# Optimization experiments

Hardware: AMD Instinct MI355X
Metric: run time of the kernel (lower is better)

The kernel has to match this reference:

```python
import jax, jax.numpy as jnp
import numpy as np

N_ETYPES = 4


def setup_inputs() -> dict:
    key = jax.random.key(0)
    ks = jax.random.split(key, 6)
    N, E, F = 50000, 800000, 128
    x = jax.random.normal(ks[0], (N, F), dtype=jnp.float32)
    edge_index = jax.random.randint(ks[1], (2, E), 0, N, dtype=jnp.int64)
    edge_type = jax.random.randint(ks[2], (E,), 0, N_ETYPES, dtype=jnp.int64)
    scale = 1.0 / np.sqrt(F)
    W_self = jax.random.normal(ks[3], (N_ETYPES, F, F), dtype=jnp.float32) * scale
    W_neigh = jax.random.normal(ks[4], (N_ETYPES, F, F), dtype=jnp.float32) * scale
    b = jnp.zeros((N_ETYPES, F), dtype=jnp.float32)
    return {"x": x, "edge_index": edge_index, "edge_type": edge_type,
            "W_self": W_self, "W_neigh": W_neigh, "b": b}


def reference(x, edge_index, edge_type, W_self, W_neigh, b):
    # HeteroConv: per-edge-type SageConv (mean aggregation), then mean over types.
    N = x.shape[0]
    src, dst = edge_index[0], edge_index[1]
    msg = x[src]                                   # [E, F] gathered source features
    outs = []
    for t in range(N_ETYPES):                      # small fixed loop over edge types
        w = (edge_type == t).astype(x.dtype)[:, None]          # [E, 1] type mask
        agg = jax.ops.segment_sum(msg * w, dst, num_segments=N)  # [N, F]
        cnt = jax.ops.segment_sum(w, dst, num_segments=N)        # [N, 1]
        mean_agg = agg / jnp.maximum(cnt, 1.0)
        outs.append(x @ W_self[t] + mean_agg @ W_neigh[t] + b[t])
    out = jnp.stack(outs, axis=0)                  # [n_etypes, N, F]
    return out.mean(axis=0)                        # reduction='mean' over edge types
```

## Files before the change

### kernel.cpp

```cpp
#include <hip/hip_runtime.h>

#define FDIM 128
#define NT 4
#define KDIM (FDIM * (NT + 1))
#define GBM 32

#define RSH 5
#define RNODES 32
#define RCAP 768
#define NBKT 128
#define CHUNK 4096

typedef __attribute__((ext_vector_type(8))) _Float16 h8v;
typedef __attribute__((ext_vector_type(4))) float f4v;

__device__ __forceinline__ unsigned short f2h(float f) {
    _Float16 h = (_Float16)f;
    return __builtin_bit_cast(unsigned short, h);
}
__device__ __forceinline__ void gload_lds16(const void* g, void* l) {
    __builtin_amdgcn_global_load_lds(
        (const __attribute__((address_space(1))) unsigned int*)g,
        (__attribute__((address_space(3))) unsigned int*)l, 16, 0, 0);
}

__global__ __launch_bounds__(256) void k_prep(
    const float* __restrict__ x, const int* __restrict__ ei,
    const int* __restrict__ et, const float* __restrict__ Wself,
    const float* __restrict__ Wneigh, const float* __restrict__ bvec,
    unsigned short* __restrict__ xh, unsigned short* __restrict__ WmixT,
    float* __restrict__ bmean, int* __restrict__ cur,
    unsigned int* __restrict__ bin, int N, int E, int NR, int nbBin, int nbX) {
    __shared__ int lcnt[2048];
    __shared__ int lpos[2048];
    const int bid = blockIdx.x;
    const int tid = threadIdx.x;

    if (bid < nbBin) {
        const int e0 = bid * CHUNK;
        for (int b = tid; b < NR; b += 256) lcnt[b] = 0;
        __syncthreads();
        int rs[16];
        unsigned int recs[16];
#pragma unroll
        for (int i = 0; i < 16; ++i) {
            int e = e0 + i * 256 + tid;
            if (e < E) {
                int src = ei[e];
                int dst = ei[E + e];
                int t = et[e];
                rs[i] = dst >> RSH;
                recs[i] = (unsigned int)src |
                          ((unsigned int)(dst & (RNODES - 1)) << 16) |
                          ((unsigned int)t << 21);
                atomicAdd(&lcnt[rs[i]], 1);
            } else { rs[i] = -1; recs[i] = 0; }
        }
        __syncthreads();
        for (int b = tid; b < NR; b += 256) {
            int c = lcnt[b];
            lpos[b] = (c > 0) ? atomicAdd(&cur[b * 16], c) : 0;
        }
        __syncthreads();
#pragma unroll
        for (int i = 0; i < 16; ++i) {
            if (rs[i] >= 0) {
                int p = atomicAdd(&lpos[rs[i]], 1);
                if (p < RCAP) bin[(size_t)rs[i] * RCAP + p] = recs[i];
            }
        }
    } else if (bid < nbBin + nbX) {
        int i = (bid - nbBin) * 256 + tid;
        int n8 = N * FDIM / 8;
        if (i < n8) {
            float4 v0 = reinterpret_cast<const float4*>(x)[i * 2];
            float4 v1 = reinterpret_cast<const float4*>(x)[i * 2 + 1];
            ushort4 o0, o1;
            o0.x = f2h(v0.x); o0.y = f2h(v0.y); o0.z = f2h(v0.z); o0.w = f2h(v0.w);
            o1.x = f2h(v1.x); o1.y = f2h(v1.y); o1.z = f2h(v1.z); o1.w = f2h(v1.w);
            reinterpret_cast<ushort4*>(xh)[i * 2] = o0;
            reinterpret_cast<ushort4*>(xh)[i * 2 + 1] = o1;
        }
    } else {
        int i = (bid - nbBin - nbX) * 256 + tid;
        if (i < KDIM * FDIM) {
            int k = i / FDIM, j = i % FDIM;
            float v;
            if (k < FDIM) {
                v = 0.25f * (Wself[(size_t)(0 * FDIM + k) * FDIM + j] +
                             Wself[(size_t)(1 * FDIM + k) * FDIM + j] +
                             Wself[(size_t)(2 * FDIM + k) * FDIM + j] +
                             Wself[(size_t)(3 * FDIM + k) * FDIM + j]);
            } else {
                int t = (k - FDIM) >> 7;
                int kk = (k - FDIM) & (FDIM - 1);
                v = 0.25f * Wneigh[((size_t)t * FDIM + kk) * FDIM + j];
            }
            WmixT[(size_t)j * KDIM + k] = f2h(v);
            if (i < FDIM)
                bmean[i] = 0.25f * (bvec[i] + bvec[FDIM + i] +
                                    bvec[2 * FDIM + i] + bvec[3 * FDIM + i]);
        }
    }
}

__global__ __launch_bounds__(256) void k_fused(
    const unsigned short* __restrict__ xh, const int* __restrict__ cur,
    const unsigned int* __restrict__ bin, const unsigned short* __restrict__ WmixT,
    const float* __restrict__ bmean, float* __restrict__ out, int N) {
    __shared__ __align__(16) char smem[18944];
    unsigned int* recs   = (unsigned int*)smem;
    int* cur2            = (int*)(smem + 3584);
    unsigned short* As   = (unsigned short*)smem;
    unsigned short* magg = (unsigned short*)smem;
    unsigned short* srcs = (unsigned short*)(smem + 8192);
    int* cnts            = (int*)(smem + 9728);
    int* boff            = (int*)(smem + 10240);
    unsigned short* Bs   = (unsigned short*)(smem + 10752);

    const int r = blockIdx.x;
    const int tid = threadIdx.x;

    int K = cur[r * 16];
    if (K > RCAP) K = RCAP;
    for (int i = tid; i < K; i += 256) recs[i] = bin[(size_t)r * RCAP + i];
    if (tid < NBKT) cnts[tid] = 0;
    __syncthreads();
    for (int i = tid; i < K; i += 256) {
        unsigned int rec = recs[i];
        int b = ((rec >> 21) << 5) | ((rec >> 16) & 31);
        atomicAdd(&cnts[b], 1);
    }
    __syncthreads();
    if (tid < 64) {
        int c0 = cnts[2 * tid], c1 = cnts[2 * tid + 1];
        int tot = c0 + c1;
        int xs = tot;
        for (int off = 1; off < 64; off <<= 1) {
            int y = __shfl_up(xs, off, 64);
            if (tid >= off) xs += y;
        }
        int excl = xs - tot;
        boff[2 * tid] = excl;
        boff[2 * tid + 1] = excl + c0;
        cur2[2 * tid] = excl;
        cur2[2 * tid + 1] = excl + c0;
    }
    __syncthreads();
    for (int i = tid; i < K; i += 256) {
        unsigned int rec = recs[i];
        int b = ((rec >> 21) << 5) | ((rec >> 16) & 31);
        int p = atomicAdd(&cur2[b], 1);
        srcs[p] = (unsigned short)(rec & 0xffffu);
    }

    const int wid = tid >> 6, lane = tid & 63;
    const int wr = wid >> 1, wc = wid & 1;
    const int n0 = r * GBM;
    const int r16 = lane & 15, kg = lane >> 4;
    const int g = tid >> 4, ln = tid & 15;

    f4v acc[4];
#pragma unroll
    for (int n = 0; n < 4; ++n) acc[n] = (f4v){0.f, 0.f, 0.f, 0.f};
    __syncthreads();

#pragma unroll 1
    for (int ks = 0; ks < 4; ++ks) {
        int k0 = ks * 32;
        if (wid < 2) {
            int row = tid >> 2, c = tid & 3;
            int cs = c ^ ((row >> 1) & 3);
            int rg = n0 + row; if (rg >= N) rg = N - 1;
            gload_lds16(xh + (size_t)rg * FDIM + k0 + cs * 8, &As[wid * 512]);
        }
#pragma unroll
        for (int p = 0; p < 2; ++p) {
            int ck = p * 256 + tid;
            int col = ck >> 2, c = ck & 3;
            int cs = c ^ ((col >> 1) & 3);
            gload_lds16(WmixT + (size_t)col * KDIM + k0 + cs * 8,
                        &Bs[(p * 4 + wid) * 512]);
        }
        __syncthreads();
        h8v af, bfr[4];
        {
            int row = wr * 16 + r16;
            af = *reinterpret_cast<const h8v*>(
                &As[row * 32 + ((kg ^ ((row >> 1) & 3)) << 3)]);
        }
#pragma unroll
        for (int n = 0; n < 4; ++n) {
            int col = wc * 64 + n * 16 + r16;
            bfr[n] = *reinterpret_cast<const h8v*>(
                &Bs[col * 32 + ((kg ^ ((col >> 1) & 3)) << 3)]);
        }
#pragma unroll
        for (int n = 0; n < 4; ++n)
            acc[n] = __builtin_amdgcn_mfma_f32_16x16x32_f16(af, bfr[n], acc[n], 0, 0, 0);
        __syncthreads();
    }

#pragma unroll 1
    for (int t = 0; t < 4; ++t) {
#pragma unroll 1
        for (int it = 0; it < 2; ++it) {
            int dl = it * 16 + g;
            int b = (t << 5) | dl;
            int dst = n0 + dl;
            if (dst < N) {
                int beg = boff[b], m = cnts[b];
                h8v a0 = (h8v)(_Float16)0.f, a1 = (h8v)(_Float16)0.f;
                h8v a2 = (h8v)(_Float16)0.f, a3 = (h8v)(_Float16)0.f;
                int i = 0;
                for (; i + 4 <= m; i += 4) {
                    int s0 = srcs[beg + i], s1 = srcs[beg + i + 1];
                    int s2 = srcs[beg + i + 2], s3 = srcs[beg + i + 3];
                    a0 += *reinterpret_cast<const h8v*>(xh + (size_t)s0 * FDIM + ln * 8);
                    a1 += *reinterpret_cast<const h8v*>(xh + (size_t)s1 * FDIM + ln * 8);
                    a2 += *reinterpret_cast<const h8v*>(xh + (size_t)s2 * FDIM + ln * 8);
                    a3 += *reinterpret_cast<const h8v*>(xh + (size_t)s3 * FDIM + ln * 8);
                }
                if (i + 2 <= m) {
                    int s0 = srcs[beg + i], s1 = srcs[beg + i + 1];
                    a0 += *reinterpret_cast<const h8v*>(xh + (size_t)s0 * FDIM + ln * 8);
                    a1 += *reinterpret_cast<const h8v*>(xh + (size_t)s1 * FDIM + ln * 8);
                    i += 2;
                }
                if (i < m) {
                    int s0 = srcs[beg + i];
                    a0 += *reinterpret_cast<const h8v*>(xh + (size_t)s0 * FDIM + ln * 8);
                }
                float rc = (m > 0) ? 1.0f / (float)m : 0.0f;
                h8v o = ((a0 + a1) + (a2 + a3)) * (_Float16)rc;
                *reinterpret_cast<h8v*>(&magg[dl * FDIM + ((ln ^ (dl & 15)) << 3)]) = o;
            }
        }
        __syncthreads();

#pragma unroll 1
        for (int ks = 0; ks < 4; ++ks) {
            int k0 = FDIM + t * FDIM + ks * 32;
#pragma unroll
            for (int p = 0; p < 2; ++p) {
                int ck = p * 256 + tid;
                int col = ck >> 2, c = ck & 3;
                int cs = c ^ ((col >> 1) & 3);
                gload_lds16(WmixT + (size_t)col * KDIM + k0 + cs * 8,
                            &Bs[(p * 4 + wid) * 512]);
            }
            __syncthreads();
            h8v af, bfr[4];
            {
                int row = wr * 16 + r16;
                af = *reinterpret_cast<const h8v*>(
                    &magg[row * FDIM + (((ks * 4 + kg) ^ (row & 15)) << 3)]);
            }
#pragma unroll
            for (int n = 0; n < 4; ++n) {
                int col = wc * 64 + n * 16 + r16;
                bfr[n] = *reinterpret_cast<const h8v*>(
                    &Bs[col * 32 + ((kg ^ ((col >> 1) & 3)) << 3)]);
            }
#pragma unroll
            for (int n = 0; n < 4; ++n)
                acc[n] = __builtin_amdgcn_mfma_f32_16x16x32_f16(af, bfr[n], acc[n], 0, 0, 0);
            __syncthreads();
        }
    }

    float bm[4];
#pragma unroll
    for (int n = 0; n < 4; ++n) bm[n] = bmean[wc * 64 + n * 16 + r16];
#pragma unroll
    for (int j = 0; j < 4; ++j) {
        int row = n0 + wr * 16 + kg * 4 + j;
        if (row < N) {
            float* o = out + (size_t)row * FDIM;
#pragma unroll
            for (int n = 0; n < 4; ++n)
                o[wc * 64 + n * 16 + r16] = acc[n][j] + bm[n];
        }
    }
}

extern "C" void kernel_launch(void* const* d_in, const int* in_sizes, int n_in,
                              void* d_out, int out_size, void* d_ws, size_t ws_size,
                              hipStream_t stream) {
    const float* x      = (const float*)d_in[0];
    const int*   ei     = (const int*)d_in[1];
    const int*   et     = (const int*)d_in[2];
    const float* Wself  = (const float*)d_in[3];
    const float* Wneigh = (const float*)d_in[4];
    const float* b      = (const float*)d_in[5];
    float* out = (float*)d_out;

    const int N = in_sizes[0] / FDIM;
    const int E = in_sizes[2];
    const int NR = (N + RNODES - 1) >> RSH;

    char* ws = (char*)d_ws;
    unsigned short* xh    = (unsigned short*)ws;
    unsigned short* WmixT = xh + (size_t)N * FDIM;
    float* bmean = (float*)(WmixT + (size_t)FDIM * KDIM);
    int* cur     = (int*)(bmean + FDIM);
    unsigned int* bin = (unsigned int*)(cur + (size_t)NR * 16);

    hipMemsetAsync(cur, 0, (size_t)NR * 16 * sizeof(int), stream);

    const int nbBin = (E + CHUNK - 1) / CHUNK;
    const int nbX   = (N * FDIM / 8 + 255) / 256;
    const int nbM   = (KDIM * FDIM + 255) / 256;

    k_prep<<<nbBin + nbX + nbM, 256, 0, stream>>>(
        x, ei, et, Wself, Wneigh, b, xh, WmixT, bmean, cur, bin,
        N, E, NR, nbBin, nbX);

    k_fused<<<NR, 256, 0, stream>>>(xh, cur, bin, WmixT, bmean, out, N);
}
```

Baseline: 87.60 us.

## Load MFMA operands directly from global memory instead of staging through LDS

```diff
diff --git a/kernel.cpp b/kernel.cpp
--- a/kernel.cpp
+++ b/kernel.cpp
@@ -17,11 +17,6 @@
 __device__ __forceinline__ unsigned short f2h(float f) {
     _Float16 h = (_Float16)f;
     return __builtin_bit_cast(unsigned short, h);
-}
-__device__ __forceinline__ void gload_lds16(const void* g, void* l) {
-    __builtin_amdgcn_global_load_lds(
-        (const __attribute__((address_space(1))) unsigned int*)g,
-        (__attribute__((address_space(3))) unsigned int*)l, 16, 0, 0);
 }
 
 __global__ __launch_bounds__(256) void k_prep(
@@ -108,15 +103,13 @@
     const unsigned short* __restrict__ xh, const int* __restrict__ cur,
     const unsigned int* __restrict__ bin, const unsigned short* __restrict__ WmixT,
     const float* __restrict__ bmean, float* __restrict__ out, int N) {
-    __shared__ __align__(16) char smem[18944];
+    __shared__ __align__(16) char smem[10752];
     unsigned int* recs   = (unsigned int*)smem;
     int* cur2            = (int*)(smem + 3584);
-    unsigned short* As   = (unsigned short*)smem;
     unsigned short* magg = (unsigned short*)smem;
     unsigned short* srcs = (unsigned short*)(smem + 8192);
     int* cnts            = (int*)(smem + 9728);
     int* boff            = (int*)(smem + 10240);
-    unsigned short* Bs   = (unsigned short*)(smem + 10752);
 
     const int r = blockIdx.x;
     const int tid = threadIdx.x;
@@ -165,40 +158,24 @@
     for (int n = 0; n < 4; ++n) acc[n] = (f4v){0.f, 0.f, 0.f, 0.f};
     __syncthreads();
 
-#pragma unroll 1
-    for (int ks = 0; ks < 4; ++ks) {
-        int k0 = ks * 32;
-        if (wid < 2) {
-            int row = tid >> 2, c = tid & 3;
-            int cs = c ^ ((row >> 1) & 3);
-            int rg = n0 + row; if (rg >= N) rg = N - 1;
-            gload_lds16(xh + (size_t)rg * FDIM + k0 + cs * 8, &As[wid * 512]);
-        }
-#pragma unroll
-        for (int p = 0; p < 2; ++p) {
-            int ck = p * 256 + tid;
-            int col = ck >> 2, c = ck & 3;
-            int cs = c ^ ((col >> 1) & 3);
-            gload_lds16(WmixT + (size_t)col * KDIM + k0 + cs * 8,
-                        &Bs[(p * 4 + wid) * 512]);
-        }
-        __syncthreads();
-        h8v af, bfr[4];
-        {
-            int row = wr * 16 + r16;
-            af = *reinterpret_cast<const h8v*>(
-                &As[row * 32 + ((kg ^ ((row >> 1) & 3)) << 3)]);
-        }
-#pragma unroll
-        for (int n = 0; n < 4; ++n) {
-            int col = wc * 64 + n * 16 + r16;
-            bfr[n] = *reinterpret_cast<const h8v*>(
-                &Bs[col * 32 + ((kg ^ ((col >> 1) & 3)) << 3)]);
-        }
-#pragma unroll
-        for (int n = 0; n < 4; ++n)
-            acc[n] = __builtin_amdgcn_mfma_f32_16x16x32_f16(af, bfr[n], acc[n], 0, 0, 0);
-        __syncthreads();
+    {
+        int rg = n0 + wr * 16 + r16; if (rg >= N) rg = N - 1;
+        const int col0 = wc * 64;
+#pragma unroll
+        for (int ks = 0; ks < 4; ++ks) {
+            h8v af = *reinterpret_cast<const h8v*>(
+                xh + (size_t)rg * FDIM + ks * 32 + kg * 8);
+            h8v bfr[4];
+#pragma unroll
+            for (int n = 0; n < 4; ++n) {
+                int col = col0 + n * 16 + r16;
+                bfr[n] = *reinterpret_cast<const h8v*>(
+                    WmixT + (size_t)col * KDIM + ks * 32 + kg * 8);
+            }
+#pragma unroll
+            for (int n = 0; n < 4; ++n)
+                acc[n] = __builtin_amdgcn_mfma_f32_16x16x32_f16(af, bfr[n], acc[n], 0, 0, 0);
+        }
     }
 
 #pragma unroll 1
@@ -238,35 +215,28 @@
         }
         __syncthreads();
 
-#pragma unroll 1
-        for (int ks = 0; ks < 4; ++ks) {
-            int k0 = FDIM + t * FDIM + ks * 32;
-#pragma unroll
-            for (int p = 0; p < 2; ++p) {
-                int ck = p * 256 + tid;
-                int col = ck >> 2, c = ck & 3;
-                int cs = c ^ ((col >> 1) & 3);
-                gload_lds16(WmixT + (size_t)col * KDIM + k0 + cs * 8,
-                            &Bs[(p * 4 + wid) * 512]);
-            }
-            __syncthreads();
-            h8v af, bfr[4];
-            {
-                int row = wr * 16 + r16;
-                af = *reinterpret_cast<const h8v*>(
-                    &magg[row * FDIM + (((ks * 4 + kg) ^ (row & 15)) << 3)]);
-            }
-#pragma unroll
-            for (int n = 0; n < 4; ++n) {
-                int col = wc * 64 + n * 16 + r16;
-                bfr[n] = *reinterpret_cast<const h8v*>(
-                    &Bs[col * 32 + ((kg ^ ((col >> 1) & 3)) << 3)]);
-            }
-#pragma unroll
-            for (int n = 0; n < 4; ++n)
-                acc[n] = __builtin_amdgcn_mfma_f32_16x16x32_f16(af, bfr[n], acc[n], 0, 0, 0);
-            __syncthreads();
-        }
+        {
+            const int row = wr * 16 + r16;
+            const int col0 = wc * 64;
+            const size_t kbase = (size_t)(FDIM + t * FDIM);
+#pragma unroll
+            for (int ks = 0; ks < 4; ++ks) {
+                int q = ks * 4 + kg;
+                h8v af = *reinterpret_cast<const h8v*>(
+                    &magg[row * FDIM + ((q ^ (row & 15)) << 3)]);
+                h8v bfr[4];
+#pragma unroll
+                for (int n = 0; n < 4; ++n) {
+                    int col = col0 + n * 16 + r16;
+                    bfr[n] = *reinterpret_cast<const h8v*>(
+                        WmixT + (size_t)col * KDIM + kbase + ks * 32 + kg * 8);
+                }
+#pragma unroll
+                for (int n = 0; n < 4; ++n)
+                    acc[n] = __builtin_amdgcn_mfma_f32_16x16x32_f16(af, bfr[n], acc[n], 0, 0, 0);
+            }
+        }
+        __syncthreads();
     }
 
     float bm[4];
```

Measured after the change: 132.6 us. 51.3% more time.
